# Optimization experiments

Hardware: AMD Instinct MI355X
Metric: run time of the kernel (lower is better)

Reference implementation:

```python
import jax, jax.numpy as jnp
import numpy as np

B, L, D, H, NL = 32, 200, 64, 2, 2
ITEM_NUM, TIME_SPAN = 50000, 365
NEG = float(-2**32 + 1)


def _ln(x, g, b, eps=1e-8):
    m = jnp.mean(x, -1, keepdims=True)
    v = jnp.mean((x - m) ** 2, -1, keepdims=True)
    return (x - m) / jnp.sqrt(v + eps) * g + b


def setup_inputs() -> dict:
    key = jax.random.key(0)
    ks = iter(jax.random.split(key, 32))
    f = lambda shape: jax.random.normal(next(ks), shape, jnp.float32) * 0.02
    item_emb = f((ITEM_NUM + 1, D)).at[0].set(0.0)  # padding_idx=0
    return dict(
        log_ids=jax.random.randint(next(ks), (B, L), 0, ITEM_NUM + 1),
        log_times=jax.random.randint(next(ks), (B, L), 0, 100_000_000),
        pos_ids=jax.random.randint(next(ks), (B, L), 1, ITEM_NUM + 1),
        neg_ids=jax.random.randint(next(ks), (B, L), 1, ITEM_NUM + 1),
        item_emb=item_emb,
        posK_emb=f((L, D)), posV_emb=f((L, D)),
        tK_emb=f((TIME_SPAN + 1, D)), tV_emb=f((TIME_SPAN + 1, D)),
        ln1_g=jnp.ones((NL, D)), ln1_b=jnp.zeros((NL, D)),
        Wq=f((NL, D, D)), bq=jnp.zeros((NL, D)),
        Wk=f((NL, D, D)), bk=jnp.zeros((NL, D)),
        Wv=f((NL, D, D)), bv=jnp.zeros((NL, D)),
        ln2_g=jnp.ones((NL, D)), ln2_b=jnp.zeros((NL, D)),
        W1=f((NL, D, D)), b1=jnp.zeros((NL, D)),
        W2=f((NL, D, D)), b2=jnp.zeros((NL, D)),
        lnf_g=jnp.ones((D,)), lnf_b=jnp.zeros((D,)),
    )


def _attention(xq, xkv, pad, cmask, tK, tV, pK, pV, Wq, bq, Wk, bk, Wv, bv):
    dh = D // H
    Q = xq @ Wq.T + bq
    K = xkv @ Wk.T + bk
    V = xkv @ Wv.T + bv
    heads = lambda t: t.reshape(B, L, H, dh).transpose(2, 0, 1, 3)  # [H,B,L,dh]
    Qh, Kh, Vh = heads(Q), heads(K), heads(V)
    pKh = pK.reshape(L, H, dh).transpose(1, 0, 2)  # [H,L,dh] (same for all b)
    pVh = pV.reshape(L, H, dh).transpose(1, 0, 2)
    tKh = tK.reshape(B, L, L, H, dh).transpose(3, 0, 1, 2, 4)  # [H,B,Lq,Lk,dh]
    tVh = tV.reshape(B, L, L, H, dh).transpose(3, 0, 1, 2, 4)
    s = jnp.einsum('hbqd,hbkd->hbqk', Qh, Kh)
    s = s + jnp.einsum('hbqd,hkd->hbqk', Qh, pKh)
    s = s + jnp.einsum('hbqkd,hbqd->hbqk', tKh, Qh)
    s = s / (dh ** 0.5)
    s = jnp.where(pad[None, :, :, None], NEG, s)  # padded query rows
    s = jnp.where(cmask[None, None, :, :], NEG, s)  # causal mask
    A = jax.nn.softmax(s, axis=-1)
    out = jnp.einsum('hbqk,hbkd->hbqd', A, Vh)
    out = out + jnp.einsum('hbqk,hkd->hbqd', A, pVh)
    out = out + jnp.einsum('hbqk,hbqkd->hbqd', A, tVh)
    return out.transpose(1, 2, 0, 3).reshape(B, L, D)


def reference(log_ids, log_times, pos_ids, neg_ids, item_emb, posK_emb, posV_emb,
              tK_emb, tV_emb, ln1_g, ln1_b, Wq, bq, Wk, bk, Wv, bv,
              ln2_g, ln2_b, W1, b1, W2, b2, lnf_g, lnf_b):
    # per-pair time-interval buckets (days, clipped to TIME_SPAN)
    dt = jnp.abs(log_times[:, :, None] - log_times[:, None, :]).astype(jnp.float32) / 86400.0
    tmat = jnp.minimum(dt, TIME_SPAN).astype(jnp.int32)
    tK = tK_emb[tmat]  # [B,L,L,D]
    tV = tV_emb[tmat]
    pad = (log_ids == 0)
    keep = (~pad)[:, :, None].astype(item_emb.dtype)
    cmask = ~jnp.tril(jnp.ones((L, L), dtype=bool))
    x = item_emb[log_ids] * (D ** 0.5) * keep
    for i in range(NL):
        q = _ln(x, ln1_g[i], ln1_b[i])
        mha = _attention(q, x, pad, cmask, tK, tV, posK_emb, posV_emb,
                         Wq[i], bq[i], Wk[i], bk[i], Wv[i], bv[i])
        x = q + mha
        x = _ln(x, ln2_g[i], ln2_b[i])
        x = x + (jax.nn.relu(x @ W1[i].T + b1[i]) @ W2[i].T + b2[i])  # 1x1 conv FFN
        x = x * keep
    feats = _ln(x, lnf_g, lnf_b)
    pos_logits = jnp.sum(feats * item_emb[pos_ids], -1)
    neg_logits = jnp.sum(feats * item_emb[neg_ids], -1)
    return pos_logits, neg_logits
```

## Files before the change

### kernel.cpp

```cpp
#include <hip/hip_runtime.h>
#include <math.h>

#define BB 32
#define LLEN 200
#define DD 64
#define HH 2
#define NLAYER 2
#define BLD (BB * LLEN * DD)
#define TSPAN1 366

__device__ inline float waveSum(float v) {
#pragma unroll
    for (int off = 32; off > 0; off >>= 1) v += __shfl_xor(v, off);
    return v;
}
__device__ inline float halfSum(float v) {
    v += __shfl_xor(v, 1);
    v += __shfl_xor(v, 2);
    v += __shfl_xor(v, 4);
    v += __shfl_xor(v, 8);
    v += __shfl_xor(v, 16);
    return v;
}
__device__ inline float halfMax(float v) {
    v = fmaxf(v, __shfl_xor(v, 1));
    v = fmaxf(v, __shfl_xor(v, 2));
    v = fmaxf(v, __shfl_xor(v, 4));
    v = fmaxf(v, __shfl_xor(v, 8));
    v = fmaxf(v, __shfl_xor(v, 16));
    return v;
}

__device__ inline void qt_tail(const float (*Qsh)[DD], const float* __restrict__ tKT,
                               float* __restrict__ Qt_g, int base) {
    int tid = threadIdx.x;
    for (int t = tid; t < TSPAN1; t += 256) {
        const float* tk = tKT + t;
        float a0 = 0, a1 = 0, a2 = 0, a3 = 0;
#pragma unroll 8
        for (int d = 0; d < 32; ++d) {
            float v = tk[d * TSPAN1];
            a0 = fmaf(v, Qsh[0][d], a0);
            a1 = fmaf(v, Qsh[1][d], a1);
            a2 = fmaf(v, Qsh[2][d], a2);
            a3 = fmaf(v, Qsh[3][d], a3);
        }
        Qt_g[(base + 0) * (2 * TSPAN1) + t] = a0;
        Qt_g[(base + 1) * (2 * TSPAN1) + t] = a1;
        Qt_g[(base + 2) * (2 * TSPAN1) + t] = a2;
        Qt_g[(base + 3) * (2 * TSPAN1) + t] = a3;
        float b0 = 0, b1 = 0, b2 = 0, b3 = 0;
#pragma unroll 8
        for (int d = 32; d < 64; ++d) {
            float v = tk[d * TSPAN1];
            b0 = fmaf(v, Qsh[0][d], b0);
            b1 = fmaf(v, Qsh[1][d], b1);
            b2 = fmaf(v, Qsh[2][d], b2);
            b3 = fmaf(v, Qsh[3][d], b3);
        }
        Qt_g[(base + 0) * (2 * TSPAN1) + TSPAN1 + t] = b0;
        Qt_g[(base + 1) * (2 * TSPAN1) + TSPAN1 + t] = b1;
        Qt_g[(base + 2) * (2 * TSPAN1) + TSPAN1 + t] = b2;
        Qt_g[(base + 3) * (2 * TSPAN1) + TSPAN1 + t] = b3;
    }
}

__global__ void transpose_kernel(const float* __restrict__ Wq,
                                 const float* __restrict__ Wk,
                                 const float* __restrict__ Wv,
                                 const float* __restrict__ W1,
                                 const float* __restrict__ W2,
                                 const float* __restrict__ tK_emb,
                                 float* __restrict__ wt,
                                 float* __restrict__ tKT) {
    int m = blockIdx.x;
    if (m < 10) {
        const float* src;
        switch (m % 5) {
            case 0: src = Wq; break;
            case 1: src = Wk; break;
            case 2: src = Wv; break;
            case 3: src = W1; break;
            default: src = W2; break;
        }
        src += (m / 5) * DD * DD;
        float* dst = wt + m * DD * DD;
        for (int e = threadIdx.x; e < DD * DD; e += 256) {
            int d = e >> 6, j = e & 63;
            dst[j * DD + d] = src[e];
        }
    } else {
        for (int e = threadIdx.x; e < TSPAN1 * DD; e += 256) {
            int t = e >> 6, d = e & 63;
            tKT[d * TSPAN1 + t] = tK_emb[e];
        }
    }
}

__global__ void ln_qkv_kernel(const int* __restrict__ log_ids,
                              const float* __restrict__ item_emb,
                              const float* __restrict__ g,
                              const float* __restrict__ bln,
                              const float* __restrict__ WqT, const float* __restrict__ bq,
                              const float* __restrict__ WkT, const float* __restrict__ bk,
                              const float* __restrict__ WvT, const float* __restrict__ bv,
                              const float* __restrict__ posK,
                              const float* __restrict__ posV,
                              const float* __restrict__ tKT,
                              float* __restrict__ q,
                              float* __restrict__ Q, float* __restrict__ K,
                              float* __restrict__ V,
                              float* __restrict__ Qt_g) {
    __shared__ float qs[4][DD], xs[4][DD], Qsh[4][DD];
    int tid = threadIdx.x;
    int wid = tid >> 6, d = tid & 63;
    int row = blockIdx.x * 4 + wid;
    int l = row % LLEN;
    int id = log_ids[row];
    float xv = (id == 0) ? 0.0f : item_emb[id * DD + d] * 8.0f;
    xs[wid][d] = xv;
    float m = waveSum(xv) * (1.0f / 64.0f);
    float c = xv - m;
    float var = waveSum(c * c) * (1.0f / 64.0f);
    float qv = (c / sqrtf(var + 1e-8f)) * g[d] + bln[d];
    qs[wid][d] = qv;
    q[row * DD + d] = qv;
    float aq = bq[d], ak = bk[d], av = bv[d];
#pragma unroll 8
    for (int j = 0; j < DD; ++j) {
        aq = fmaf(qs[wid][j], WqT[j * DD + d], aq);
        ak = fmaf(xs[wid][j], WkT[j * DD + d], ak);
        av = fmaf(xs[wid][j], WvT[j * DD + d], av);
    }
    Q[row * DD + d] = aq;
    K[row * DD + d] = ak + posK[l * DD + d];
    V[row * DD + d] = av + posV[l * DD + d];
    Qsh[wid][d] = aq;
    __syncthreads();
    qt_tail(Qsh, tKT, Qt_g, blockIdx.x * 4);
}

__global__ void attn_kernel(const float* __restrict__ Q,
                            const float* __restrict__ Keff,
                            const float* __restrict__ Veff,
                            const int* __restrict__ log_times,
                            const float* __restrict__ Qt_g,
                            const float* __restrict__ tV_emb,
                            float* __restrict__ out) {
    __shared__ int t_s[LLEN];
    __shared__ float sc[4][HH][LLEN];
    __shared__ unsigned short tm_s[4][LLEN];
    __shared__ float qt_s[4][2 * TSPAN1];

    int tid = threadIdx.x;
    int wid = tid >> 6;
    int lane = tid & 63;
    int bi = blockIdx.x / 50;
    int i = blockIdx.x % 50;
    int qi = (wid == 0) ? i : (wid == 1) ? (99 - i) : (wid == 2) ? (100 + i) : (199 - i);
    int row = bi * LLEN + qi;
    int len = qi + 1;

    if (tid < LLEN) t_s[tid] = log_times[bi * LLEN + tid];
    __syncthreads();

    const float* qtrow_g = Qt_g + row * (2 * TSPAN1);
    for (int e = lane; e < 2 * TSPAN1; e += 64) qt_s[wid][e] = qtrow_g[e];

    int tq = t_s[qi];
    for (int k = lane; k < len; k += 64) {
        int dt = tq - t_s[k];
        if (dt < 0) dt = -dt;
        float dtf = fminf((float)dt * (1.0f / 86400.0f), 365.0f);
        tm_s[wid][k] = (unsigned short)(int)dtf;
    }

    int h = lane >> 5;
    int l5 = lane & 31;
    int cch = l5 >> 2;
    int jo = l5 & 3;
    float4 qv = ((const float4*)(Q + row * DD))[h * 8 + cch];
    const float4* K4 = (const float4*)(Keff + bi * LLEN * DD);
    const float scale = 0.17677669529663687f;

    for (int k0 = 0; k0 < len; k0 += 4) {
        int k = k0 + jo;
        int kc = (k < len) ? k : (len - 1);
        int bucket = tm_s[wid][kc];
        float4 kv = K4[kc * 16 + h * 8 + cch];
        float p = qv.x * kv.x + qv.y * kv.y + qv.z * kv.z + qv.w * kv.w;
        p += __shfl_xor(p, 4);
        p += __shfl_xor(p, 8);
        p += __shfl_xor(p, 16);
        float s = (p + qt_s[wid][h * TSPAN1 + bucket]) * scale;
        if (cch == 0 && k < len) sc[wid][h][k] = s;
    }

    {
        float m = -INFINITY;
        for (int k = l5; k < len; k += 32) m = fmaxf(m, sc[wid][h][k]);
        m = halfMax(m);
        float s = 0.0f;
        for (int k = l5; k < len; k += 32) {
            float e = expf(sc[wid][h][k] - m);
            sc[wid][h][k] = e;
            s += e;
        }
        s = halfSum(s);
        float inv = 1.0f / s;
        for (int k = l5; k < len; k += 32) sc[wid][h][k] *= inv;
    }

    const float* Vb = Veff + bi * LLEN * DD + lane;
    const float* tVl = tV_emb + lane;
    float acc0 = 0.0f, acc1 = 0.0f, acc2 = 0.0f, acc3 = 0.0f;
    int k = 0;
    for (; k + 4 <= len; k += 4) {
        int b0 = tm_s[wid][k + 0];
        int b1 = tm_s[wid][k + 1];
        int b2 = tm_s[wid][k + 2];
        int b3 = tm_s[wid][k + 3];
        float a0 = sc[wid][h][k + 0];
        float a1 = sc[wid][h][k + 1];
        float a2 = sc[wid][h][k + 2];
        float a3 = sc[wid][h][k + 3];
        acc0 = fmaf(a0, Vb[(k + 0) * DD] + tVl[b0 * DD], acc0);
        acc1 = fmaf(a1, Vb[(k + 1) * DD] + tVl[b1 * DD], acc1);
        acc2 = fmaf(a2, Vb[(k + 2) * DD] + tVl[b2 * DD], acc2);
        acc3 = fmaf(a3, Vb[(k + 3) * DD] + tVl[b3 * DD], acc3);
    }
    for (; k < len; ++k) {
        int b0 = tm_s[wid][k];
        acc0 = fmaf(sc[wid][h][k], Vb[k * DD] + tVl[b0 * DD], acc0);
    }
    out[row * DD + lane] = (acc0 + acc1) + (acc2 + acc3);
}

__global__ void mid_kernel(const float* __restrict__ qin,
                           const float* __restrict__ att,
                           const float* __restrict__ g2, const float* __restrict__ b2ln,
                           const float* __restrict__ W1T, const float* __restrict__ b1v,
                           const float* __restrict__ W2T, const float* __restrict__ b2v,
                           const int* __restrict__ log_ids,
                           const float* __restrict__ g1n, const float* __restrict__ b1n,
                           const float* __restrict__ WqT, const float* __restrict__ bq,
                           const float* __restrict__ WkT, const float* __restrict__ bk,
                           const float* __restrict__ WvT, const float* __restrict__ bv,
                           const float* __restrict__ posK,
                           const float* __restrict__ posV,
                           const float* __restrict__ tKT,
                           float* __restrict__ q,
                           float* __restrict__ Q, float* __restrict__ K,
                           float* __restrict__ V,
                           float* __restrict__ Qt_g) {
    __shared__ float xs[4][DD], hs[4][DD], qs[4][DD], Qsh[4][DD];
    int tid = threadIdx.x;
    int wid = tid >> 6, d = tid & 63;
    int row = blockIdx.x * 4 + wid;
    int l = row % LLEN;
    float v = qin[row * DD + d] + att[row * DD + d];
    float m = waveSum(v) * (1.0f / 64.0f);
    float c = v - m;
    float var = waveSum(c * c) * (1.0f / 64.0f);
    float xv = (c / sqrtf(var + 1e-8f)) * g2[d] + b2ln[d];
    xs[wid][d] = xv;
    float a = b1v[d];
#pragma unroll 8
    for (int j = 0; j < DD; ++j) a = fmaf(xs[wid][j], W1T[j * DD + d], a);
    hs[wid][d] = fmaxf(a, 0.0f);
    float o = b2v[d];
#pragma unroll 8
    for (int j = 0; j < DD; ++j) o = fmaf(hs[wid][j], W2T[j * DD + d], o);
    float res = xv + o;
    if (log_ids[row] == 0) res = 0.0f;
    float m2 = waveSum(res) * (1.0f / 64.0f);
    float c2 = res - m2;
    float var2 = waveSum(c2 * c2) * (1.0f / 64.0f);
    float qv = (c2 / sqrtf(var2 + 1e-8f)) * g1n[d] + b1n[d];
    qs[wid][d] = qv;
    xs[wid][d] = res;
    q[row * DD + d] = qv;
    float aq = bq[d], ak = bk[d], av = bv[d];
#pragma unroll 8
    for (int j = 0; j < DD; ++j) {
        aq = fmaf(qs[wid][j], WqT[j * DD + d], aq);
        ak = fmaf(xs[wid][j], WkT[j * DD + d], ak);
        av = fmaf(xs[wid][j], WvT[j * DD + d], av);
    }
    Q[row * DD + d] = aq;
    K[row * DD + d] = ak + posK[l * DD + d];
    V[row * DD + d] = av + posV[l * DD + d];
    Qsh[wid][d] = aq;
    __syncthreads();
    qt_tail(Qsh, tKT, Qt_g, blockIdx.x * 4);
}

__global__ void end_kernel(const float* __restrict__ qin,
                           const float* __restrict__ att,
                           const float* __restrict__ g2, const float* __restrict__ b2ln,
                           const float* __restrict__ W1T, const float* __restrict__ b1v,
                           const float* __restrict__ W2T, const float* __restrict__ b2v,
                           const int* __restrict__ log_ids,
                           const float* __restrict__ lnf_g, const float* __restrict__ lnf_b,
                           const float* __restrict__ item_emb,
                           const int* __restrict__ pos_ids,
                           const int* __restrict__ neg_ids,
                           float* __restrict__ out) {
    __shared__ float xs[4][DD], hs[4][DD];
    int tid = threadIdx.x;
    int wid = tid >> 6, d = tid & 63;
    int row = blockIdx.x * 4 + wid;
    float v = qin[row * DD + d] + att[row * DD + d];
    float m = waveSum(v) * (1.0f / 64.0f);
    float c = v - m;
    float var = waveSum(c * c) * (1.0f / 64.0f);
    float xv = (c / sqrtf(var + 1e-8f)) * g2[d] + b2ln[d];
    xs[wid][d] = xv;
    float a = b1v[d];
#pragma unroll 8
    for (int j = 0; j < DD; ++j) a = fmaf(xs[wid][j], W1T[j * DD + d], a);
    hs[wid][d] = fmaxf(a, 0.0f);
    float o = b2v[d];
#pragma unroll 8
    for (int j = 0; j < DD; ++j) o = fmaf(hs[wid][j], W2T[j * DD + d], o);
    float res = xv + o;
    if (log_ids[row] == 0) res = 0.0f;
    float m2 = waveSum(res) * (1.0f / 64.0f);
    float c2 = res - m2;
    float var2 = waveSum(c2 * c2) * (1.0f / 64.0f);
    float f = (c2 / sqrtf(var2 + 1e-8f)) * lnf_g[d] + lnf_b[d];
    int pid = pos_ids[row];
    int nid = neg_ids[row];
    float p = waveSum(f * item_emb[pid * DD + d]);
    float n = waveSum(f * item_emb[nid * DD + d]);
    if (d == 0) {
        out[row] = p;
        out[BB * LLEN + row] = n;
    }
}

extern "C" void kernel_launch(void* const* d_in, const int* in_sizes, int n_in,
                              void* d_out, int out_size, void* d_ws, size_t ws_size,
                              hipStream_t stream) {
    const int* log_ids = (const int*)d_in[0];
    const int* log_times = (const int*)d_in[1];
    const int* pos_ids = (const int*)d_in[2];
    const int* neg_ids = (const int*)d_in[3];
    const float* item_emb = (const float*)d_in[4];
    const float* posK = (const float*)d_in[5];
    const float* posV = (const float*)d_in[6];
    const float* tK_emb = (const float*)d_in[7];
    const float* tV_emb = (const float*)d_in[8];
    const float* ln1_g = (const float*)d_in[9];
    const float* ln1_b = (const float*)d_in[10];
    const float* Wq = (const float*)d_in[11];
    const float* bq = (const float*)d_in[12];
    const float* Wk = (const float*)d_in[13];
    const float* bk = (const float*)d_in[14];
    const float* Wv = (const float*)d_in[15];
    const float* bv = (const float*)d_in[16];
    const float* ln2_g = (const float*)d_in[17];
    const float* ln2_b = (const float*)d_in[18];
    const float* W1 = (const float*)d_in[19];
    const float* b1 = (const float*)d_in[20];
    const float* W2 = (const float*)d_in[21];
    const float* b2 = (const float*)d_in[22];
    const float* lnf_g = (const float*)d_in[23];
    const float* lnf_b = (const float*)d_in[24];

    float* ws = (float*)d_ws;
    float* q = ws;
    float* Qb = q + BLD;
    float* Kb = Qb + BLD;
    float* Vb = Kb + BLD;
    float* att = Vb + BLD;
    float* wt = att + BLD;
    float* tKT = wt + 10 * DD * DD;
    float* Qt = tKT + DD * TSPAN1;

    const int nrow = BB * LLEN;

    const float* W1T0 = wt + 3 * DD * DD;
    const float* W2T0 = wt + 4 * DD * DD;
    const float* W1T1 = wt + 8 * DD * DD;
    const float* W2T1 = wt + 9 * DD * DD;

    transpose_kernel<<<11, 256, 0, stream>>>(Wq, Wk, Wv, W1, W2, tK_emb, wt, tKT);

    ln_qkv_kernel<<<nrow / 4, 256, 0, stream>>>(log_ids, item_emb,
                                                ln1_g, ln1_b,
                                                wt + 0 * DD * DD, bq,
                                                wt + 1 * DD * DD, bk,
                                                wt + 2 * DD * DD, bv,
                                                posK, posV, tKT,
                                                q, Qb, Kb, Vb, Qt);
    attn_kernel<<<BB * 50, 256, 0, stream>>>(Qb, Kb, Vb, log_times, Qt, tV_emb, att);

    mid_kernel<<<nrow / 4, 256, 0, stream>>>(q, att,
                                             ln2_g, ln2_b,
                                             W1T0, b1, W2T0, b2,
                                             log_ids,
                                             ln1_g + DD, ln1_b + DD,
                                             wt + 5 * DD * DD, bq + DD,
                                             wt + 6 * DD * DD, bk + DD,
                                             wt + 7 * DD * DD, bv + DD,
                                             posK, posV, tKT,
                                             q, Qb, Kb, Vb, Qt);
    attn_kernel<<<BB * 50, 256, 0, stream>>>(Qb, Kb, Vb, log_times, Qt, tV_emb, att);

    end_kernel<<<nrow / 4, 256, 0, stream>>>(q, att,
                                             ln2_g + DD, ln2_b + DD,
                                             W1T1, b1 + DD, W2T1, b2 + DD,
                                             log_ids,
                                             lnf_g, lnf_b, item_emb,
                                             pos_ids, neg_ids, (float*)d_out);
}
```

Baseline: 183.3 us.

## Vectorize attention kernel loads: float4 Qt copy, softmax, and float2 PV accumulation

The attention kernel now copies the Qt row with float4 loads and runs the softmax on two float4 chunks per lane, with the shared-memory arrays padded and aligned for this. The P·V loop is restructured so each half-wave handles alternate keys with float2 loads of V and tV, and the two halves are combined with a cross-lane shuffle. The goal is fewer memory instructions and fewer shared-memory accesses. The cost is extra shuffles, select logic, and lanes that compute only masked values in the softmax.

```diff
diff --git a/kernel.cpp b/kernel.cpp
--- a/kernel.cpp
+++ b/kernel.cpp
@@ -148,9 +148,9 @@
                             const float* __restrict__ tV_emb,
                             float* __restrict__ out) {
     __shared__ int t_s[LLEN];
-    __shared__ float sc[4][HH][LLEN];
-    __shared__ unsigned short tm_s[4][LLEN];
-    __shared__ float qt_s[4][2 * TSPAN1];
+    __shared__ __align__(16) float sc[4][HH][256];
+    __shared__ __align__(16) unsigned short tm_s[4][208];
+    __shared__ __align__(16) float qt_s[4][2 * TSPAN1];
 
     int tid = threadIdx.x;
     int wid = tid >> 6;
@@ -164,8 +164,11 @@
     if (tid < LLEN) t_s[tid] = log_times[bi * LLEN + tid];
     __syncthreads();
 
-    const float* qtrow_g = Qt_g + row * (2 * TSPAN1);
-    for (int e = lane; e < 2 * TSPAN1; e += 64) qt_s[wid][e] = qtrow_g[e];
+    {
+        const float4* qtrow4 = (const float4*)(Qt_g + (size_t)row * (2 * TSPAN1));
+        float4* qts4 = (float4*)&qt_s[wid][0];
+        for (int e = lane; e < 183; e += 64) qts4[e] = qtrow4[e];
+    }
 
     int tq = t_s[qi];
     for (int k = lane; k < len; k += 64) {
@@ -180,7 +183,7 @@
     int cch = l5 >> 2;
     int jo = l5 & 3;
     float4 qv = ((const float4*)(Q + row * DD))[h * 8 + cch];
-    const float4* K4 = (const float4*)(Keff + bi * LLEN * DD);
+    const float4* K4 = (const float4*)(Keff + (size_t)bi * LLEN * DD);
     const float scale = 0.17677669529663687f;
 
     for (int k0 = 0; k0 < len; k0 += 4) {
@@ -197,43 +200,78 @@
     }
 
     {
+        int b1 = 4 * l5, b2 = 128 + 4 * l5;
+        float4 f1 = *(const float4*)&sc[wid][h][b1];
+        float4 f2 = *(const float4*)&sc[wid][h][b2];
         float m = -INFINITY;
-        for (int k = l5; k < len; k += 32) m = fmaxf(m, sc[wid][h][k]);
+        if (b1 + 0 < len) m = fmaxf(m, f1.x);
+        if (b1 + 1 < len) m = fmaxf(m, f1.y);
+        if (b1 + 2 < len) m = fmaxf(m, f1.z);
+        if (b1 + 3 < len) m = fmaxf(m, f1.w);
+        if (b2 + 0 < len) m = fmaxf(m, f2.x);
+        if (b2 + 1 < len) m = fmaxf(m, f2.y);
+        if (b2 + 2 < len) m = fmaxf(m, f2.z);
+        if (b2 + 3 < len) m = fmaxf(m, f2.w);
         m = halfMax(m);
-        float s = 0.0f;
-        for (int k = l5; k < len; k += 32) {
-            float e = expf(sc[wid][h][k] - m);
-            sc[wid][h][k] = e;
-            s += e;
-        }
+        float4 e1, e2;
+        e1.x = (b1 + 0 < len) ? expf(f1.x - m) : 0.0f;
+        e1.y = (b1 + 1 < len) ? expf(f1.y - m) : 0.0f;
+        e1.z = (b1 + 2 < len) ? expf(f1.z - m) : 0.0f;
+        e1.w = (b1 + 3 < len) ? expf(f1.w - m) : 0.0f;
+        e2.x = (b2 + 0 < len) ? expf(f2.x - m) : 0.0f;
+        e2.y = (b2 + 1 < len) ? expf(f2.y - m) : 0.0f;
+        e2.z = (b2 + 2 < len) ? expf(f2.z - m) : 0.0f;
+        e2.w = (b2 + 3 < len) ? expf(f2.w - m) : 0.0f;
+        float s = ((e1.x + e1.y) + (e1.z + e1.w)) + ((e2.x + e2.y) + (e2.z + e2.w));
         s = halfSum(s);
         float inv = 1.0f / s;
-        for (int k = l5; k < len; k += 32) sc[wid][h][k] *= inv;
-    }
-
-    const float* Vb = Veff + bi * LLEN * DD + lane;
-    const float* tVl = tV_emb + lane;
-    float acc0 = 0.0f, acc1 = 0.0f, acc2 = 0.0f, acc3 = 0.0f;
+        e1.x *= inv; e1.y *= inv; e1.z *= inv; e1.w *= inv;
+        e2.x *= inv; e2.y *= inv; e2.z *= inv; e2.w *= inv;
+        *(float4*)&sc[wid][h][b1] = e1;
+        *(float4*)&sc[wid][h][b2] = e2;
+    }
+
+    const float2* V2 = (const float2*)(Veff + (size_t)bi * LLEN * DD);
+    const float2* tV2 = (const float2*)tV_emb;
+    int l5x = lane & 31;
+    int kh = lane >> 5;
+    int h2 = l5x >> 4;
+    float acc0x = 0, acc0y = 0, acc1x = 0, acc1y = 0;
     int k = 0;
     for (; k + 4 <= len; k += 4) {
-        int b0 = tm_s[wid][k + 0];
-        int b1 = tm_s[wid][k + 1];
-        int b2 = tm_s[wid][k + 2];
-        int b3 = tm_s[wid][k + 3];
-        float a0 = sc[wid][h][k + 0];
-        float a1 = sc[wid][h][k + 1];
-        float a2 = sc[wid][h][k + 2];
-        float a3 = sc[wid][h][k + 3];
-        acc0 = fmaf(a0, Vb[(k + 0) * DD] + tVl[b0 * DD], acc0);
-        acc1 = fmaf(a1, Vb[(k + 1) * DD] + tVl[b1 * DD], acc1);
-        acc2 = fmaf(a2, Vb[(k + 2) * DD] + tVl[b2 * DD], acc2);
-        acc3 = fmaf(a3, Vb[(k + 3) * DD] + tVl[b3 * DD], acc3);
-    }
-    for (; k < len; ++k) {
-        int b0 = tm_s[wid][k];
-        acc0 = fmaf(sc[wid][h][k], Vb[k * DD] + tVl[b0 * DD], acc0);
-    }
-    out[row * DD + lane] = (acc0 + acc1) + (acc2 + acc3);
+        float4 a4 = *(const float4*)&sc[wid][h2][k];
+        ushort4 t4 = *(const ushort4*)&tm_s[wid][k];
+        float aA = kh ? a4.y : a4.x;
+        float aB = kh ? a4.w : a4.z;
+        int bA = kh ? (int)t4.y : (int)t4.x;
+        int bB = kh ? (int)t4.w : (int)t4.z;
+        float2 v0 = V2[(k + kh) * 32 + l5x];
+        float2 tv0 = tV2[bA * 32 + l5x];
+        float2 v1 = V2[(k + 2 + kh) * 32 + l5x];
+        float2 tv1 = tV2[bB * 32 + l5x];
+        acc0x = fmaf(aA, v0.x + tv0.x, acc0x);
+        acc0y = fmaf(aA, v0.y + tv0.y, acc0y);
+        acc1x = fmaf(aB, v1.x + tv1.x, acc1x);
+        acc1y = fmaf(aB, v1.y + tv1.y, acc1y);
+    }
+    if (kh == 0) {
+        for (; k < len; ++k) {
+            float a = sc[wid][h2][k];
+            int b = tm_s[wid][k];
+            float2 vv = V2[k * 32 + l5x];
+            float2 tv = tV2[b * 32 + l5x];
+            acc0x = fmaf(a, vv.x + tv.x, acc0x);
+            acc0y = fmaf(a, vv.y + tv.y, acc0y);
+        }
+    }
+    float ox = acc0x + acc1x;
+    float oy = acc0y + acc1y;
+    ox += __shfl_xor(ox, 32);
+    oy += __shfl_xor(oy, 32);
+    if (kh == 0) {
+        float2 o2; o2.x = ox; o2.y = oy;
+        *(float2*)&out[row * DD + 2 * l5x] = o2;
+    }
 }
 
 __global__ void mid_kernel(const float* __restrict__ qin,
```

Measured after the change: 191.1 us. +4.2%, slower.

## Drop weight/tK transpose kernel and read row-major weights with float4 dot products

Applied to the files above, without the earlier changes.

Removes the preprocessing kernel that transposed the projection, FFN and time-key embedding matrices. Projections and the Q·tK table are now computed by reading each output row's weights directly as float4 vectors. This saves one kernel launch and the scratch writes it made. In exchange, lanes in a wave read weight rows 256 bytes apart, so loads are less coalesced than the old transposed column reads.

```diff
diff --git a/kernel.cpp b/kernel.cpp
--- a/kernel.cpp
+++ b/kernel.cpp
@@ -31,32 +31,65 @@
     return v;
 }
 
-__device__ inline void qt_tail(const float (*Qsh)[DD], const float* __restrict__ tKT,
+__device__ inline float rowdot(const float* __restrict__ W, int d,
+                               const float* __restrict__ xsrc, float acc) {
+    const float4* Wr = (const float4*)(W + d * DD);
+    const float4* xr = (const float4*)xsrc;
+#pragma unroll
+    for (int jj = 0; jj < 16; ++jj) {
+        float4 w4 = Wr[jj];
+        float4 x4 = xr[jj];
+        acc = fmaf(w4.x, x4.x, acc);
+        acc = fmaf(w4.y, x4.y, acc);
+        acc = fmaf(w4.z, x4.z, acc);
+        acc = fmaf(w4.w, x4.w, acc);
+    }
+    return acc;
+}
+
+__device__ inline void qt_tail(const float (*Qsh)[DD],
+                               const float* __restrict__ tK_emb,
                                float* __restrict__ Qt_g, int base) {
     int tid = threadIdx.x;
     for (int t = tid; t < TSPAN1; t += 256) {
-        const float* tk = tKT + t;
+        const float4* tk4 = (const float4*)(tK_emb + t * DD);
         float a0 = 0, a1 = 0, a2 = 0, a3 = 0;
-#pragma unroll 8
-        for (int d = 0; d < 32; ++d) {
-            float v = tk[d * TSPAN1];
-            a0 = fmaf(v, Qsh[0][d], a0);
-            a1 = fmaf(v, Qsh[1][d], a1);
-            a2 = fmaf(v, Qsh[2][d], a2);
-            a3 = fmaf(v, Qsh[3][d], a3);
+#pragma unroll
+        for (int dd = 0; dd < 8; ++dd) {
+            float4 v = tk4[dd];
+            const float4 q0 = *(const float4*)&Qsh[0][dd * 4];
+            const float4 q1 = *(const float4*)&Qsh[1][dd * 4];
+            const float4 q2 = *(const float4*)&Qsh[2][dd * 4];
+            const float4 q3 = *(const float4*)&Qsh[3][dd * 4];
+            a0 = fmaf(v.x, q0.x, a0); a0 = fmaf(v.y, q0.y, a0);
+            a0 = fmaf(v.z, q0.z, a0); a0 = fmaf(v.w, q0.w, a0);
+            a1 = fmaf(v.x, q1.x, a1); a1 = fmaf(v.y, q1.y, a1);
+            a1 = fmaf(v.z, q1.z, a1); a1 = fmaf(v.w, q1.w, a1);
+            a2 = fmaf(v.x, q2.x, a2); a2 = fmaf(v.y, q2.y, a2);
+            a2 = fmaf(v.z, q2.z, a2); a2 = fmaf(v.w, q2.w, a2);
+            a3 = fmaf(v.x, q3.x, a3); a3 = fmaf(v.y, q3.y, a3);
+            a3 = fmaf(v.z, q3.z, a3); a3 = fmaf(v.w, q3.w, a3);
         }
         Qt_g[(base + 0) * (2 * TSPAN1) + t] = a0;
         Qt_g[(base + 1) * (2 * TSPAN1) + t] = a1;
         Qt_g[(base + 2) * (2 * TSPAN1) + t] = a2;
         Qt_g[(base + 3) * (2 * TSPAN1) + t] = a3;
         float b0 = 0, b1 = 0, b2 = 0, b3 = 0;
-#pragma unroll 8
-        for (int d = 32; d < 64; ++d) {
-            float v = tk[d * TSPAN1];
-            b0 = fmaf(v, Qsh[0][d], b0);
-            b1 = fmaf(v, Qsh[1][d], b1);
-            b2 = fmaf(v, Qsh[2][d], b2);
-            b3 = fmaf(v, Qsh[3][d], b3);
+#pragma unroll
+        for (int dd = 8; dd < 16; ++dd) {
+            float4 v = tk4[dd];
+            const float4 q0 = *(const float4*)&Qsh[0][dd * 4];
+            const float4 q1 = *(const float4*)&Qsh[1][dd * 4];
+            const float4 q2 = *(const float4*)&Qsh[2][dd * 4];
+            const float4 q3 = *(const float4*)&Qsh[3][dd * 4];
+            b0 = fmaf(v.x, q0.x, b0); b0 = fmaf(v.y, q0.y, b0);
+            b0 = fmaf(v.z, q0.z, b0); b0 = fmaf(v.w, q0.w, b0);
+            b1 = fmaf(v.x, q1.x, b1); b1 = fmaf(v.y, q1.y, b1);
+            b1 = fmaf(v.z, q1.z, b1); b1 = fmaf(v.w, q1.w, b1);
+            b2 = fmaf(v.x, q2.x, b2); b2 = fmaf(v.y, q2.y, b2);
+            b2 = fmaf(v.z, q2.z, b2); b2 = fmaf(v.w, q2.w, b2);
+            b3 = fmaf(v.x, q3.x, b3); b3 = fmaf(v.y, q3.y, b3);
+            b3 = fmaf(v.z, q3.z, b3); b3 = fmaf(v.w, q3.w, b3);
         }
         Qt_g[(base + 0) * (2 * TSPAN1) + TSPAN1 + t] = b0;
         Qt_g[(base + 1) * (2 * TSPAN1) + TSPAN1 + t] = b1;
@@ -65,48 +98,16 @@
     }
 }
 
-__global__ void transpose_kernel(const float* __restrict__ Wq,
-                                 const float* __restrict__ Wk,
-                                 const float* __restrict__ Wv,
-                                 const float* __restrict__ W1,
-                                 const float* __restrict__ W2,
-                                 const float* __restrict__ tK_emb,
-                                 float* __restrict__ wt,
-                                 float* __restrict__ tKT) {
-    int m = blockIdx.x;
-    if (m < 10) {
-        const float* src;
-        switch (m % 5) {
-            case 0: src = Wq; break;
-            case 1: src = Wk; break;
-            case 2: src = Wv; break;
-            case 3: src = W1; break;
-            default: src = W2; break;
-        }
-        src += (m / 5) * DD * DD;
-        float* dst = wt + m * DD * DD;
-        for (int e = threadIdx.x; e < DD * DD; e += 256) {
-            int d = e >> 6, j = e & 63;
-            dst[j * DD + d] = src[e];
-        }
-    } else {
-        for (int e = threadIdx.x; e < TSPAN1 * DD; e += 256) {
-            int t = e >> 6, d = e & 63;
-            tKT[d * TSPAN1 + t] = tK_emb[e];
-        }
-    }
-}
-
 __global__ void ln_qkv_kernel(const int* __restrict__ log_ids,
                               const float* __restrict__ item_emb,
                               const float* __restrict__ g,
                               const float* __restrict__ bln,
-                              const float* __restrict__ WqT, const float* __restrict__ bq,
-                              const float* __restrict__ WkT, const float* __restrict__ bk,
-                              const float* __restrict__ WvT, const float* __restrict__ bv,
+                              const float* __restrict__ Wq, const float* __restrict__ bq,
+                              const float* __restrict__ Wk, const float* __restrict__ bk,
+                              const float* __restrict__ Wv, const float* __restrict__ bv,
                               const float* __restrict__ posK,
                               const float* __restrict__ posV,
-                              const float* __restrict__ tKT,
+                              const float* __restrict__ tK_emb,
                               float* __restrict__ q,
                               float* __restrict__ Q, float* __restrict__ K,
                               float* __restrict__ V,
@@ -125,19 +126,15 @@
     float qv = (c / sqrtf(var + 1e-8f)) * g[d] + bln[d];
     qs[wid][d] = qv;
     q[row * DD + d] = qv;
-    float aq = bq[d], ak = bk[d], av = bv[d];
-#pragma unroll 8
-    for (int j = 0; j < DD; ++j) {
-        aq = fmaf(qs[wid][j], WqT[j * DD + d], aq);
-        ak = fmaf(xs[wid][j], WkT[j * DD + d], ak);
-        av = fmaf(xs[wid][j], WvT[j * DD + d], av);
-    }
+    float aq = rowdot(Wq, d, qs[wid], bq[d]);
+    float ak = rowdot(Wk, d, xs[wid], bk[d]);
+    float av = rowdot(Wv, d, xs[wid], bv[d]);
     Q[row * DD + d] = aq;
     K[row * DD + d] = ak + posK[l * DD + d];
     V[row * DD + d] = av + posV[l * DD + d];
     Qsh[wid][d] = aq;
     __syncthreads();
-    qt_tail(Qsh, tKT, Qt_g, blockIdx.x * 4);
+    qt_tail(Qsh, tK_emb, Qt_g, blockIdx.x * 4);
 }
 
 __global__ void attn_kernel(const float* __restrict__ Q,
@@ -164,7 +161,7 @@
     if (tid < LLEN) t_s[tid] = log_times[bi * LLEN + tid];
     __syncthreads();
 
-    const float* qtrow_g = Qt_g + row * (2 * TSPAN1);
+    const float* qtrow_g = Qt_g + (size_t)row * (2 * TSPAN1);
     for (int e = lane; e < 2 * TSPAN1; e += 64) qt_s[wid][e] = qtrow_g[e];
 
     int tq = t_s[qi];
@@ -180,7 +177,7 @@
     int cch = l5 >> 2;
     int jo = l5 & 3;
     float4 qv = ((const float4*)(Q + row * DD))[h * 8 + cch];
-    const float4* K4 = (const float4*)(Keff + bi * LLEN * DD);
+    const float4* K4 = (const float4*)(Keff + (size_t)bi * LLEN * DD);
     const float scale = 0.17677669529663687f;
 
     for (int k0 = 0; k0 < len; k0 += 4) {
@@ -211,7 +208,7 @@
         for (int k = l5; k < len; k += 32) sc[wid][h][k] *= inv;
     }
 
-    const float* Vb = Veff + bi * LLEN * DD + lane;
+    const float* Vb = Veff + (size_t)bi * LLEN * DD + lane;
     const float* tVl = tV_emb + lane;
     float acc0 = 0.0f, acc1 = 0.0f, acc2 = 0.0f, acc3 = 0.0f;
     int k = 0;
@@ -239,16 +236,16 @@
 __global__ void mid_kernel(const float* __restrict__ qin,
                            const float* __restrict__ att,
                            const float* __restrict__ g2, const float* __restrict__ b2ln,
-                           const float* __restrict__ W1T, const float* __restrict__ b1v,
-                           const float* __restrict__ W2T, const float* __restrict__ b2v,
+                           const float* __restrict__ W1, const float* __restrict__ b1v,
+                           const float* __restrict__ W2, const float* __restrict__ b2v,
                            const int* __restrict__ log_ids,
                            const float* __restrict__ g1n, const float* __restrict__ b1n,
-                           const float* __restrict__ WqT, const float* __restrict__ bq,
-                           const float* __restrict__ WkT, const float* __restrict__ bk,
-                           const float* __restrict__ WvT, const float* __restrict__ bv,
+                           const float* __restrict__ Wq, const float* __restrict__ bq,
+                           const float* __restrict__ Wk, const float* __restrict__ bk,
+                           const float* __restrict__ Wv, const float* __restrict__ bv,
                            const float* __restrict__ posK,
                            const float* __restrict__ posV,
-                           const float* __restrict__ tKT,
+                           const float* __restrict__ tK_emb,
                            float* __restrict__ q,
                            float* __restrict__ Q, float* __restrict__ K,
                            float* __restrict__ V,
@@ -264,13 +261,9 @@
     float var = waveSum(c * c) * (1.0f / 64.0f);
     float xv = (c / sqrtf(var + 1e-8f)) * g2[d] + b2ln[d];
     xs[wid][d] = xv;
-    float a = b1v[d];
-#pragma unroll 8
-    for (int j = 0; j < DD; ++j) a = fmaf(xs[wid][j], W1T[j * DD + d], a);
+    float a = rowdot(W1, d, xs[wid], b1v[d]);
     hs[wid][d] = fmaxf(a, 0.0f);
-    float o = b2v[d];
-#pragma unroll 8
-    for (int j = 0; j < DD; ++j) o = fmaf(hs[wid][j], W2T[j * DD + d], o);
+    float o = rowdot(W2, d, hs[wid], b2v[d]);
     float res = xv + o;
     if (log_ids[row] == 0) res = 0.0f;
     float m2 = waveSum(res) * (1.0f / 64.0f);
@@ -280,26 +273,22 @@
     qs[wid][d] = qv;
     xs[wid][d] = res;
     q[row * DD + d] = qv;
-    float aq = bq[d], ak = bk[d], av = bv[d];
-#pragma unroll 8
-    for (int j = 0; j < DD; ++j) {
-        aq = fmaf(qs[wid][j], WqT[j * DD + d], aq);
-        ak = fmaf(xs[wid][j], WkT[j * DD + d], ak);
-        av = fmaf(xs[wid][j], WvT[j * DD + d], av);
-    }
+    float aq = rowdot(Wq, d, qs[wid], bq[d]);
+    float ak = rowdot(Wk, d, xs[wid], bk[d]);
+    float av = rowdot(Wv, d, xs[wid], bv[d]);
     Q[row * DD + d] = aq;
     K[row * DD + d] = ak + posK[l * DD + d];
     V[row * DD + d] = av + posV[l * DD + d];
     Qsh[wid][d] = aq;
     __syncthreads();
-    qt_tail(Qsh, tKT, Qt_g, blockIdx.x * 4);
+    qt_tail(Qsh, tK_emb, Qt_g, blockIdx.x * 4);
 }
 
 __global__ void end_kernel(const float* __restrict__ qin,
                            const float* __restrict__ att,
                            const float* __restrict__ g2, const float* __restrict__ b2ln,
-                           const float* __restrict__ W1T, const float* __restrict__ b1v,
-                           const float* __restrict__ W2T, const float* __restrict__ b2v,
+                           const float* __restrict__ W1, const float* __restrict__ b1v,
+                           const float* __restrict__ W2, const float* __restrict__ b2v,
                            const int* __restrict__ log_ids,
                            const float* __restrict__ lnf_g, const float* __restrict__ lnf_b,
                            const float* __restrict__ item_emb,
@@ -316,13 +305,9 @@
     float var = waveSum(c * c) * (1.0f / 64.0f);
     float xv = (c / sqrtf(var + 1e-8f)) * g2[d] + b2ln[d];
     xs[wid][d] = xv;
-    float a = b1v[d];
-#pragma unroll 8
-    for (int j = 0; j < DD; ++j) a = fmaf(xs[wid][j], W1T[j * DD + d], a);
+    float a = rowdot(W1, d, xs[wid], b1v[d]);
     hs[wid][d] = fmaxf(a, 0.0f);
-    float o = b2v[d];
-#pragma unroll 8
-    for (int j = 0; j < DD; ++j) o = fmaf(hs[wid][j], W2T[j * DD + d], o);
+    float o = rowdot(W2, d, hs[wid], b2v[d]);
     float res = xv + o;
     if (log_ids[row] == 0) res = 0.0f;
     float m2 = waveSum(res) * (1.0f / 64.0f);
@@ -374,43 +359,33 @@
     float* Kb = Qb + BLD;
     float* Vb = Kb + BLD;
     float* att = Vb + BLD;
-    float* wt = att + BLD;
-    float* tKT = wt + 10 * DD * DD;
-    float* Qt = tKT + DD * TSPAN1;
+    float* Qt = att + BLD;
 
     const int nrow = BB * LLEN;
-
-    const float* W1T0 = wt + 3 * DD * DD;
-    const float* W2T0 = wt + 4 * DD * DD;
-    const float* W1T1 = wt + 8 * DD * DD;
-    const float* W2T1 = wt + 9 * DD * DD;
-
-    transpose_kernel<<<11, 256, 0, stream>>>(Wq, Wk, Wv, W1, W2, tK_emb, wt, tKT);
+    const int DD2 = DD * DD;
 
     ln_qkv_kernel<<<nrow / 4, 256, 0, stream>>>(log_ids, item_emb,
                                                 ln1_g, ln1_b,
-                                                wt + 0 * DD * DD, bq,
-                                                wt + 1 * DD * DD, bk,
-                                                wt + 2 * DD * DD, bv,
-                                                posK, posV, tKT,
+                                                Wq, bq, Wk, bk, Wv, bv,
+                                                posK, posV, tK_emb,
                                                 q, Qb, Kb, Vb, Qt);
     attn_kernel<<<BB * 50, 256, 0, stream>>>(Qb, Kb, Vb, log_times, Qt, tV_emb, att);
 
     mid_kernel<<<nrow / 4, 256, 0, stream>>>(q, att,
                                              ln2_g, ln2_b,
-                                             W1T0, b1, W2T0, b2,
+                                             W1, b1, W2, b2,
                                              log_ids,
                                              ln1_g + DD, ln1_b + DD,
-                                             wt + 5 * DD * DD, bq + DD,
-                                             wt + 6 * DD * DD, bk + DD,
-                                             wt + 7 * DD * DD, bv + DD,
-                                             posK, posV, tKT,
+                                             Wq + DD2, bq + DD,
+                                             Wk + DD2, bk + DD,
+                                             Wv + DD2, bv + DD,
+                                             posK, posV, tK_emb,
                                              q, Qb, Kb, Vb, Qt);
     attn_kernel<<<BB * 50, 256, 0, stream>>>(Qb, Kb, Vb, log_times, Qt, tV_emb, att);
 
     end_kernel<<<nrow / 4, 256, 0, stream>>>(q, att,
                                              ln2_g + DD, ln2_b + DD,
-                                             W1T1, b1 + DD, W2T1, b2 + DD,
+                                             W1 + DD2, b1 + DD, W2 + DD2, b2 + DD,
                                              log_ids,
                                              lnf_g, lnf_b, item_emb,
                                              pos_ids, neg_ids, (float*)d_out);
```

New measurement: 462.4 us. 2.52x slower.
